# Optimization experiments

Measured on AMD Instinct MI355X. Metric: run time of the kernel, lower is better.

## Reference

```python
import jax, jax.numpy as jnp
import numpy as np

D = 256; NH = 8; NL = 4; NP = 4; HD = D // NH
SHAPES = np.array([[180, 180], [90, 90], [45, 45], [23, 23]], dtype=np.int32)
LQ = int((SHAPES[:, 0] * SHAPES[:, 1]).sum())  # 43054
STARTS = np.concatenate([[0], np.cumsum(SHAPES[:, 0] * SHAPES[:, 1])[:-1]]).astype(np.int32)


def setup_inputs():
    ks = jax.random.split(jax.random.key(0), 16)
    s = 0.02
    p = lambda k, shp: jax.random.normal(k, shp, jnp.float32) * s
    return {
        "query": jax.random.normal(ks[0], (1, LQ, D), jnp.float32),
        "ref_points": jax.random.uniform(ks[1], (1, LQ, NL, 2), dtype=jnp.float32),
        "pos": jax.random.normal(ks[2], (1, LQ, D), jnp.float32),
        "input_spatial_shapes": jnp.asarray(SHAPES),
        "input_level_start_index": jnp.asarray(STARTS),
        "w_off": p(ks[3], (D, NH * NL * NP * 2)), "b_off": p(ks[4], (NH * NL * NP * 2,)),
        "w_attn": p(ks[5], (D, NH * NL * NP)), "b_attn": p(ks[6], (NH * NL * NP,)),
        "w_val": p(ks[7], (D, D)), "b_val": jnp.zeros((D,), jnp.float32),
        "w_out": p(ks[8], (D, D)), "b_out": jnp.zeros((D,), jnp.float32),
        "g1": jnp.ones((D,), jnp.float32), "beta1": jnp.zeros((D,), jnp.float32),
        "w1": p(ks[9], (D, D)), "b1": jnp.zeros((D,), jnp.float32),
        "w2": p(ks[10], (D, D)), "b2": jnp.zeros((D,), jnp.float32),
        "g2": jnp.ones((D,), jnp.float32), "beta2": jnp.zeros((D,), jnp.float32),
    }


def _ln(x, g, b):
    m = x.mean(-1, keepdims=True)
    v = ((x - m) ** 2).mean(-1, keepdims=True)
    return (x - m) * jax.lax.rsqrt(v + 1e-5) * g + b


def _sample_level(v, Hl, Wl, loc):
    # v: (B, Hl*Wl, NH, HD); loc: (B, Lq, NH, NP, 2) normalized to [0,1]
    # Bilinear sampling matching F.grid_sample(align_corners=False, padding_mode='zeros')
    B, _, nh, d = v.shape
    Lq, P = loc.shape[1], loc.shape[3]
    vb = jnp.transpose(v, (0, 2, 1, 3))  # (B, NH, HW, d)
    x = loc[..., 0] * Wl - 0.5
    y = loc[..., 1] * Hl - 0.5
    x0 = jnp.floor(x); y0 = jnp.floor(y)
    fx = x - x0; fy = y - y0
    out = jnp.zeros((B, nh, Lq, P, d), v.dtype)
    for dy in (0, 1):
        for dx in (0, 1):
            xi = x0 + dx; yi = y0 + dy
            w = (fx if dx else 1.0 - fx) * (fy if dy else 1.0 - fy)
            valid = (xi >= 0) & (xi < Wl) & (yi >= 0) & (yi < Hl)
            xc = jnp.clip(xi, 0, Wl - 1).astype(jnp.int32)
            yc = jnp.clip(yi, 0, Hl - 1).astype(jnp.int32)
            idx = jnp.transpose(yc * Wl + xc, (0, 2, 1, 3)).reshape(B, nh, Lq * P)
            g = jnp.take_along_axis(vb, idx[..., None], axis=2).reshape(B, nh, Lq, P, d)
            wt = jnp.transpose(jnp.where(valid, w, 0.0), (0, 2, 1, 3))
            out = out + g * wt[..., None]
    return out  # (B, NH, Lq, NP, HD)


def _layer(query, ref_points, pos, shp, sti, w_off, b_off, w_attn, b_attn, w_val, b_val,
           w_out, b_out, g1, beta1, w1, b1, w2, b2, g2, beta2):
    B, Lq, _ = query.shape
    q = query + pos  # with_pos_embed
    value = (query @ w_val + b_val).reshape(B, Lq, NH, HD)
    off = (q @ w_off + b_off).reshape(B, Lq, NH, NL, NP, 2)
    aw = jax.nn.softmax((q @ w_attn + b_attn).reshape(B, Lq, NH, NL * NP), axis=-1)
    aw = aw.reshape(B, Lq, NH, NL, NP)
    # offset_normalizer = [W_l, H_l]
    norm = jnp.asarray(shp[:, ::-1].copy(), jnp.float32)
    loc = ref_points[:, :, None, :, None, :] + off / norm[None, None, None, :, None, :]
    acc = jnp.zeros((B, NH, Lq, HD), query.dtype)
    for l in range(NL):
        Hl, Wl = int(shp[l, 0]), int(shp[l, 1])
        st = int(sti[l])
        sampled = _sample_level(value[:, st:st + Hl * Wl], Hl, Wl, loc[:, :, :, l])
        wl = jnp.transpose(aw[:, :, :, l], (0, 2, 1, 3))  # (B, NH, Lq, NP)
        acc = acc + (sampled * wl[..., None]).sum(axis=3)
    attn_out = acc.transpose(0, 2, 1, 3).reshape(B, Lq, D) @ w_out + b_out
    # residual + LayerNorm + FFN (dropout is identity in eval mode)
    x = _ln(query + attn_out, g1, beta1)
    ffn = jax.nn.relu(x @ w1 + b1) @ w2 + b2
    return _ln(x + ffn, g2, beta2)


def reference(query, ref_points, pos, input_spatial_shapes, input_level_start_index,
              w_off, b_off, w_attn, b_attn, w_val, b_val, w_out, b_out,
              g1, beta1, w1, b1, w2, b2, g2, beta2):
    shp = np.asarray(input_spatial_shapes)
    sti = np.asarray(input_level_start_index)
    return _layer(query, ref_points, pos, shp, sti, w_off, b_off, w_attn, b_attn,
                  w_val, b_val, w_out, b_out, g1, beta1, w1, b1, w2, b2, g2, beta2)
```

## Files before the change

kernel.cpp:

```cpp
#include <hip/hip_runtime.h>

typedef unsigned short u16;
typedef unsigned int u32;
typedef float f32x4 __attribute__((ext_vector_type(4)));
typedef short i16x8 __attribute__((ext_vector_type(8)));
typedef __bf16 bf16x8_t __attribute__((ext_vector_type(8)));

#define LQ 43054

__device__ __forceinline__ float bf2f(u16 u) {
  union { u32 i; float f; } v; v.i = ((u32)u) << 16; return v.f;
}
__device__ __forceinline__ u16 f2bf(float f) {
  u32 i = __float_as_uint(f);
  return (u16)((i + 0x7FFFu + ((i >> 16) & 1u)) >> 16);
}

template <typename T>
__device__ __forceinline__ auto mfma_try(T a, T b, f32x4 c, int)
    -> decltype(__builtin_amdgcn_mfma_f32_16x16x32_bf16(a, b, c, 0, 0, 0)) {
  return __builtin_amdgcn_mfma_f32_16x16x32_bf16(a, b, c, 0, 0, 0);
}
template <typename T>
__device__ __forceinline__ f32x4 mfma_try(T a, T b, f32x4 c, long) {
  return __builtin_amdgcn_mfma_f32_16x16x32_bf16(
      __builtin_bit_cast(bf16x8_t, a), __builtin_bit_cast(bf16x8_t, b), c, 0, 0, 0);
}
__device__ __forceinline__ f32x4 mfma_bf16(i16x8 a, i16x8 b, f32x4 c) {
  return mfma_try(a, b, c, 0);
}

__global__ void transpose_all_kernel(
    const float* __restrict__ w_off, const float* __restrict__ w_attn,
    const float* __restrict__ w_val, const float* __restrict__ w_out,
    const float* __restrict__ w1, const float* __restrict__ w2,
    u16* __restrict__ wT) {
  int b = blockIdx.x;
  const float* src; u16* dst; int N; int col;
  if (b < 256)       { src = w_off;  dst = wT;          N = 256; col = b; }
  else if (b < 384)  { src = w_attn; dst = wT + 65536;  N = 128; col = b - 256; }
  else if (b < 640)  { src = w_val;  dst = wT + 98304;  N = 256; col = b - 384; }
  else if (b < 896)  { src = w_out;  dst = wT + 163840; N = 256; col = b - 640; }
  else if (b < 1152) { src = w1;     dst = wT + 229376; N = 256; col = b - 896; }
  else               { src = w2;     dst = wT + 294912; N = 256; col = b - 1152; }
  dst[col * 256 + threadIdx.x] = f2bf(src[threadIdx.x * N + col]);
}

__device__ __forceinline__ void stage_a_bf16(uint4* As, const u16* A, int r0, int M, int tid) {
#pragma unroll
  for (int it = 0; it < 8; ++it) {
    int e = tid + it * 256;
    int row = e >> 5, c = e & 31;
    int gr = r0 + row;
    uint4 v = make_uint4(0u, 0u, 0u, 0u);
    if (gr < M) v = ((const uint4*)A)[gr * 32 + c];
    As[row * 32 + (c ^ (row & 7))] = v;
  }
}
template <int ADD>
__device__ __forceinline__ void stage_a_f32(uint4* As, const float* A, const float* A2,
                                            int r0, int M, int tid) {
#pragma unroll
  for (int it = 0; it < 16; ++it) {
    int e = tid + it * 256;
    int row = e >> 6, c4 = e & 63;
    int gr = r0 + row;
    float4 v = make_float4(0.f, 0.f, 0.f, 0.f);
    if (gr < M) {
      v = ((const float4*)A)[gr * 64 + c4];
      if constexpr (ADD) {
        float4 p = ((const float4*)A2)[gr * 64 + c4];
        v.x += p.x; v.y += p.y; v.z += p.z; v.w += p.w;
      }
    }
    uint2 pk;
    pk.x = (u32)f2bf(v.x) | ((u32)f2bf(v.y) << 16);
    pk.y = (u32)f2bf(v.z) | ((u32)f2bf(v.w) << 16);
    int c = c4 >> 1, hf = c4 & 1;
    ((uint2*)As)[((row * 32 + (c ^ (row & 7))) << 1) | hf] = pk;
  }
}
__device__ __forceinline__ void load_b(i16x8* f, const u16* Bt, int t, int l16, int quad) {
  const uint4* bp = (const uint4*)Bt + (t * 16 + l16) * 32 + quad;
#pragma unroll
  for (int kk = 0; kk < 8; ++kk) f[kk] = __builtin_bit_cast(i16x8, bp[kk << 2]);
}
__device__ __forceinline__ void tile_mfma(f32x4* acc, const uint4* As,
                                          const i16x8* bfr, int l16, int quad) {
#pragma unroll
  for (int rg = 0; rg < 4; ++rg) {
    int arow = rg * 16 + l16;
    f32x4 a = {0.f, 0.f, 0.f, 0.f};
#pragma unroll
    for (int kk = 0; kk < 8; ++kk) {
      i16x8 afr = __builtin_bit_cast(i16x8, As[arow * 32 + (((kk << 2) + quad) ^ (arow & 7))]);
      a = mfma_bf16(afr, bfr[kk], a);
    }
    acc[rg] = a;
  }
}

#define LS_STRIDE 264
__device__ __forceinline__ void lds_store_rows(const u16* Ls, u16* out,
                                               int r0, int M, int w, int lane) {
#pragma unroll
  for (int it = 0; it < 8; ++it) {
    int lrow = w * 16 + it * 2 + (lane >> 5);
    int grow = r0 + lrow;
    int chunk = lane & 31;
    if (grow < M) {
      *(uint4*)(out + (size_t)grow * 256 + chunk * 8) =
          *(const uint4*)(Ls + lrow * LS_STRIDE + chunk * 8);
    }
  }
}

template <int AIN, int MODE, int NT>
__global__ __launch_bounds__(256, 3) void gemm_kernel(
    const void* __restrict__ Av, const u16* __restrict__ Bt,
    const float* __restrict__ bias, void* __restrict__ out, int M) {
  __shared__ uint4 As[2176];
  const int tid = threadIdx.x;
  const int w = tid >> 6, lane = tid & 63, quad = lane >> 4, l16 = lane & 15;
  const int r0 = blockIdx.x * 64;
  if constexpr (AIN == 2) stage_a_bf16(As, (const u16*)Av, r0, M, tid);
  else                    stage_a_f32<0>(As, (const float*)Av, nullptr, r0, M, tid);
  __syncthreads();
  i16x8 bfr[2][8];
  load_b(bfr[0], Bt, w * 4, l16, quad);
  f32x4 vals[4][4];
#pragma unroll
  for (int i = 0; i < 4; ++i) {
    const int t = w * 4 + i;
    if (i + 1 < 4) load_b(bfr[(i + 1) & 1], Bt, t + 1, l16, quad);
    tile_mfma(vals[i], As, bfr[i & 1], l16, quad);
  }
  __syncthreads();
  u16* Ls = (u16*)As;
#pragma unroll
  for (int i = 0; i < 4; ++i) {
    const int col = (w * 4 + i) * 16 + l16;
    const float bv = bias[col];
#pragma unroll
    for (int rg = 0; rg < 4; ++rg)
#pragma unroll
      for (int r = 0; r < 4; ++r) {
        float v = vals[i][rg][r] + bv;
        if (MODE == 2) v = fmaxf(v, 0.f);
        Ls[(rg * 16 + (quad << 2) + r) * LS_STRIDE + col] = f2bf(v);
      }
  }
  __syncthreads();
  lds_store_rows(Ls, (u16*)out, r0, M, w, lane);
}

__global__ __launch_bounds__(256, 3) void offaw_gemm_kernel(
    const float* __restrict__ query, const float* __restrict__ pos,
    const u16* __restrict__ Bt, const float* __restrict__ b_off,
    const float* __restrict__ b_attn, u16* __restrict__ offb,
    float* __restrict__ aw, int M) {
  __shared__ uint4 As[2176];
  const int tid = threadIdx.x;
  const int w = tid >> 6, lane = tid & 63, quad = lane >> 4, l16 = lane & 15;
  const int r0 = blockIdx.x * 64;
  stage_a_f32<1>(As, query, pos, r0, M, tid);
  __syncthreads();
  i16x8 bfr[2][8];
  load_b(bfr[0], Bt, w, l16, quad);
  f32x4 vals[4][4];
#pragma unroll
  for (int i = 0; i < 6; ++i) {
    const int t = w + 4 * i;
    if (i + 1 < 6) load_b(bfr[(i + 1) & 1], Bt, w + 4 * (i + 1), l16, quad);
    if (i < 4) {
      tile_mfma(vals[i], As, bfr[i & 1], l16, quad);
    } else {
      f32x4 acc[4];
      tile_mfma(acc, As, bfr[i & 1], l16, quad);
      const int colc = (t - 16) * 16 + l16;
      const float bv = b_attn[colc];
#pragma unroll
      for (int rg = 0; rg < 4; ++rg)
#pragma unroll
        for (int r = 0; r < 4; ++r) {
          float v = acc[rg][r] + bv;
          float m = v;
#pragma unroll
          for (int o = 1; o < 16; o <<= 1) m = fmaxf(m, __shfl_xor(m, o));
          float e = __expf(v - m);
          float s = e;
#pragma unroll
          for (int o = 1; o < 16; o <<= 1) s += __shfl_xor(s, o);
          int row = r0 + rg * 16 + (quad << 2) + r;
          if (row < M) aw[row * 128 + colc] = e / s;
        }
    }
  }
  __syncthreads();
  u16* Ls = (u16*)As;
#pragma unroll
  for (int i = 0; i < 4; ++i) {
    const int col = (w + 4 * i) * 16 + l16;
    const float bv = b_off[col];
#pragma unroll
    for (int rg = 0; rg < 4; ++rg)
#pragma unroll
      for (int r = 0; r < 4; ++r)
        Ls[(rg * 16 + (quad << 2) + r) * LS_STRIDE + col] = f2bf(vals[i][rg][r] + bv);
  }
  __syncthreads();
  lds_store_rows(Ls, offb, r0, M, w, lane);
}

template <int RBF, int OBF>
__global__ __launch_bounds__(256, 2) void gemm_ln_kernel(
    const u16* __restrict__ A, const u16* __restrict__ Bt,
    const float* __restrict__ bias, const void* __restrict__ residv,
    const float* __restrict__ g, const float* __restrict__ beta,
    void* __restrict__ outv, int M) {
  __shared__ uint4 As[2176];
  __shared__ float2 pnorm[256];
  const int tid = threadIdx.x;
  const int w = tid >> 6, lane = tid & 63, quad = lane >> 4, l16 = lane & 15;
  const int r0 = blockIdx.x * 64;
  stage_a_bf16(As, A, r0, M, tid);
  __syncthreads();
  i16x8 bfr[2][8];
  load_b(bfr[0], Bt, w * 4, l16, quad);
  f32x4 vals[4][4];
#pragma unroll
  for (int i = 0; i < 4; ++i) {
    const int t = w * 4 + i;
    if (i + 1 < 4) load_b(bfr[(i + 1) & 1], Bt, t + 1, l16, quad);
    tile_mfma(vals[i], As, bfr[i & 1], l16, quad);
  }
  float s[16], s2[16];
#pragma unroll
  for (int k = 0; k < 16; ++k) { s[k] = 0.f; s2[k] = 0.f; }
#pragma unroll
  for (int i = 0; i < 4; ++i) {
    const int col = (w * 4 + i) * 16 + l16;
    const float bv = bias[col];
#pragma unroll
    for (int rg = 0; rg < 4; ++rg)
#pragma unroll
      for (int r = 0; r < 4; ++r) {
        int row = r0 + rg * 16 + (quad << 2) + r;
        float rv = 0.f;
        if (row < M) rv = RBF ? bf2f(((const u16*)residv)[row * 256 + col])
                              : ((const float*)residv)[row * 256 + col];
        float v = vals[i][rg][r] + bv + rv;
        vals[i][rg][r] = v;
        s[rg * 4 + r] += v; s2[rg * 4 + r] += v * v;
      }
  }
#pragma unroll
  for (int k = 0; k < 16; ++k)
#pragma unroll
    for (int o = 1; o < 16; o <<= 1) {
      s[k] += __shfl_xor(s[k], o);
      s2[k] += __shfl_xor(s2[k], o);
    }
  if (l16 == 0) {
#pragma unroll
    for (int rg = 0; rg < 4; ++rg)
#pragma unroll
      for (int r = 0; r < 4; ++r) {
        int lrow = rg * 16 + (quad << 2) + r;
        pnorm[lrow * 4 + w] = make_float2(s[rg * 4 + r], s2[rg * 4 + r]);
      }
  }
  __syncthreads();
  if constexpr (OBF) {
    u16* Ls = (u16*)As;
#pragma unroll
    for (int rg = 0; rg < 4; ++rg)
#pragma unroll
      for (int r = 0; r < 4; ++r) {
        int lrow = rg * 16 + (quad << 2) + r;
        float4 p01 = ((const float4*)pnorm)[lrow * 2];
        float4 p23 = ((const float4*)pnorm)[lrow * 2 + 1];
        float ss = p01.x + p01.z + p23.x + p23.z;
        float qq = p01.y + p01.w + p23.y + p23.w;
        float mean = ss * (1.f / 256.f);
        float var = qq * (1.f / 256.f) - mean * mean;
        float inv = rsqrtf(var + 1e-5f);
#pragma unroll
        for (int i = 0; i < 4; ++i) {
          const int col = (w * 4 + i) * 16 + l16;
          float o = (vals[i][rg][r] - mean) * inv * g[col] + beta[col];
          Ls[lrow * LS_STRIDE + col] = f2bf(o);
        }
      }
    __syncthreads();
    lds_store_rows(Ls, (u16*)outv, r0, M, w, lane);
  } else {
#pragma unroll
    for (int rg = 0; rg < 4; ++rg)
#pragma unroll
      for (int r = 0; r < 4; ++r) {
        int lrow = rg * 16 + (quad << 2) + r;
        float4 p01 = ((const float4*)pnorm)[lrow * 2];
        float4 p23 = ((const float4*)pnorm)[lrow * 2 + 1];
        float ss = p01.x + p01.z + p23.x + p23.z;
        float qq = p01.y + p01.w + p23.y + p23.w;
        float mean = ss * (1.f / 256.f);
        float var = qq * (1.f / 256.f) - mean * mean;
        float inv = rsqrtf(var + 1e-5f);
        int row = r0 + lrow;
        if (row < M) {
#pragma unroll
          for (int i = 0; i < 4; ++i) {
            const int col = (w * 4 + i) * 16 + l16;
            float o = (vals[i][rg][r] - mean) * inv * g[col] + beta[col];
            ((float*)outv)[row * 256 + col] = o;
          }
        }
      }
  }
}

__global__ __launch_bounds__(256) void sampler_kernel(
    const float* __restrict__ refp, const u16* __restrict__ offb,
    const float* __restrict__ aw, const u16* __restrict__ value,
    u32* __restrict__ accv) {
  __shared__ uint4 rec[272];
  const int t = threadIdx.x;
  const int b = blockIdx.x;
  {
    const int qs = t >> 7, j = t & 127;
    const int i = b * 2 + qs;
    const int h = j >> 4, lp = j & 15, l = lp >> 2;
    const int Wl = (l == 0) ? 180 : (l == 1) ? 90 : (l == 2) ? 45 : 23;
    const int st = (l == 0) ? 0 : (l == 1) ? 32400 : (l == 2) ? 40500 : 42525;
    const float wj = aw[i * 128 + j];
    const u32 o2 = *(const u32*)(offb + i * 256 + h * 32 + lp * 2);
    const float ox = bf2f((u16)(o2 & 0xffffu)), oy = bf2f((u16)(o2 >> 16));
    const float rx = refp[i * 8 + l * 2], ry = refp[i * 8 + l * 2 + 1];
    float x = rx * (float)Wl + ox - 0.5f;
    float y = ry * (float)Wl + oy - 0.5f;
    float x0f = floorf(x), y0f = floorf(y);
    float fx = x - x0f, fy = y - y0f;
    int x0 = (int)x0f, y0 = (int)y0f;
    bool vx0 = (x0 >= 0) & (x0 < Wl), vx1 = (x0 + 1 >= 0) & (x0 + 1 < Wl);
    bool vy0 = (y0 >= 0) & (y0 < Wl), vy1 = (y0 + 1 >= 0) & (y0 + 1 < Wl);
    int x0c = min(max(x0, 0), Wl - 1), x1c = min(max(x0 + 1, 0), Wl - 1);
    int y0c = min(max(y0, 0), Wl - 1), y1c = min(max(y0 + 1, 0), Wl - 1);
    float w00 = (vx0 & vy0) ? wj * (1.f - fx) * (1.f - fy) : 0.f;
    float w01 = (vx1 & vy0) ? wj * fx * (1.f - fy) : 0.f;
    float w10 = (vx0 & vy1) ? wj * (1.f - fx) * fy : 0.f;
    float w11 = (vx1 & vy1) ? wj * fx * fy : 0.f;
    uint4 r;
    r.x = (u32)((st + y0c * Wl + x0c) * 512 + h * 64) | (u32)(x1c - x0c);
    r.y = (u32)(y1c - y0c) * (u32)(Wl * 512);
    r.z = (u32)f2bf(w00) | ((u32)f2bf(w01) << 16);
    r.w = (u32)f2bf(w10) | ((u32)f2bf(w11) << 16);
    rec[qs * 136 + h * 17 + lp] = r;
  }
  __syncthreads();
  const int qs = t >> 7, j = t & 127;
  const int h = j >> 4, dp = j & 15;
  const char* vb = (const char*)value;
  float a0 = 0.f, a1 = 0.f;
  const int rbase = qs * 136 + h * 17;
#pragma unroll
  for (int p = 0; p < 16; ++p) {
    uint4 r = rec[rbase + p];
    u32 base = (r.x & 0xFFFFFFFEu) + (u32)(dp * 4);
    u32 dxo = (r.x & 1u) << 9;
    u32 dyo = r.y;
    float w00 = __uint_as_float(r.z << 16);
    float w01 = __uint_as_float(r.z & 0xFFFF0000u);
    float w10 = __uint_as_float(r.w << 16);
    float w11 = __uint_as_float(r.w & 0xFFFF0000u);
    u32 p00 = *(const u32*)(vb + base);
    u32 p01 = *(const u32*)(vb + base + dxo);
    u32 p10 = *(const u32*)(vb + base + dyo);
    u32 p11 = *(const u32*)(vb + base + dyo + dxo);
    a0 = fmaf(w00, __uint_as_float(p00 << 16), a0);
    a1 = fmaf(w00, __uint_as_float(p00 & 0xFFFF0000u), a1);
    a0 = fmaf(w01, __uint_as_float(p01 << 16), a0);
    a1 = fmaf(w01, __uint_as_float(p01 & 0xFFFF0000u), a1);
    a0 = fmaf(w10, __uint_as_float(p10 << 16), a0);
    a1 = fmaf(w10, __uint_as_float(p10 & 0xFFFF0000u), a1);
    a0 = fmaf(w11, __uint_as_float(p11 << 16), a0);
    a1 = fmaf(w11, __uint_as_float(p11 & 0xFFFF0000u), a1);
  }
  u32 pk = (u32)f2bf(a0) | ((u32)f2bf(a1) << 16);
  accv[(b * 2 + qs) * 128 + j] = pk;
}

extern "C" void kernel_launch(void* const* d_in, const int* in_sizes, int n_in,
                              void* d_out, int out_size, void* d_ws, size_t ws_size,
                              hipStream_t stream) {
  const float* query  = (const float*)d_in[0];
  const float* refp   = (const float*)d_in[1];
  const float* pos    = (const float*)d_in[2];
  const float* w_off  = (const float*)d_in[5];
  const float* b_off  = (const float*)d_in[6];
  const float* w_attn = (const float*)d_in[7];
  const float* b_attn = (const float*)d_in[8];
  const float* w_val  = (const float*)d_in[9];
  const float* b_val  = (const float*)d_in[10];
  const float* w_out  = (const float*)d_in[11];
  const float* b_out  = (const float*)d_in[12];
  const float* g1     = (const float*)d_in[13];
  const float* beta1  = (const float*)d_in[14];
  const float* w1     = (const float*)d_in[15];
  const float* b1     = (const float*)d_in[16];
  const float* w2     = (const float*)d_in[17];
  const float* b2     = (const float*)d_in[18];
  const float* g2     = (const float*)d_in[19];
  const float* beta2  = (const float*)d_in[20];

  char* ws = (char*)d_ws;
  u16*   wT    = (u16*)(ws + 0);
  u16*   value = (u16*)(ws + 720896);
  u16*   offb  = (u16*)(ws + 22764544);
  float* aw    = (float*)(ws + 44808192);
  u16*   accb  = (u16*)(ws + 66851840);
  u16*   xb    = (u16*)(ws + 720896);
  u16*   hb    = (u16*)(ws + 22764544);

  u16* woffT  = wT;
  u16* wvalT  = wT + 98304;
  u16* woutT  = wT + 163840;
  u16* w1T    = wT + 229376;
  u16* w2T    = wT + 294912;

  transpose_all_kernel<<<1408, 256, 0, stream>>>(w_off, w_attn, w_val, w_out, w1, w2, wT);

  const int gm = (LQ + 63) / 64;
  gemm_kernel<0, 1, 4><<<gm, 256, 0, stream>>>(query, wvalT, b_val, value, LQ);
  offaw_gemm_kernel<<<gm, 256, 0, stream>>>(query, pos, woffT, b_off, b_attn, offb, aw, LQ);
  sampler_kernel<<<LQ / 2, 256, 0, stream>>>(refp, offb, aw, value, (u32*)accb);
  gemm_ln_kernel<0, 1><<<gm, 256, 0, stream>>>(accb, woutT, b_out, query, g1, beta1, xb, LQ);
  gemm_kernel<2, 2, 4><<<gm, 256, 0, stream>>>(xb, w1T, b1, hb, LQ);
  gemm_ln_kernel<1, 0><<<gm, 256, 0, stream>>>(hb, w2T, b2, xb, g2, beta2, d_out, LQ);
}
```

Before: 423.1 us.

## Use direct global-to-LDS loads, batch f32 staging loads, and dot2 bf16 sampling

The bf16 A-tile staging in the GEMM kernels now uses global_load_lds, which writes to shared memory without passing through registers. The swizzle is applied on the global address side, and out-of-range rows are clamped to the last row instead of zero-filled. The f32 staging path issues all loads of a phase before converting, so more loads are in flight at once. The sampler's bilinear accumulation now uses v_dot2_f32_bf16 with byte permutes instead of eight unpack-and-FMA steps per point. This trades some accumulation precision and adds reliance on the DMA path's layout matching the swizzle.

```diff
diff --git a/kernel.cpp b/kernel.cpp
--- a/kernel.cpp
+++ b/kernel.cpp
@@ -14,6 +14,12 @@
 __device__ __forceinline__ u16 f2bf(float f) {
   u32 i = __float_as_uint(f);
   return (u16)((i + 0x7FFFu + ((i >> 16) & 1u)) >> 16);
+}
+
+__device__ __forceinline__ float dot2bf(u32 v, u32 w, float c) {
+  float d;
+  asm("v_dot2_f32_bf16 %0, %1, %2, %3" : "=v"(d) : "v"(v), "v"(w), "v"(c));
+  return d;
 }
 
 template <typename T>
@@ -46,38 +52,50 @@
   dst[col * 256 + threadIdx.x] = f2bf(src[threadIdx.x * N + col]);
 }
 
-__device__ __forceinline__ void stage_a_bf16(uint4* As, const u16* A, int r0, int M, int tid) {
-#pragma unroll
-  for (int it = 0; it < 8; ++it) {
-    int e = tid + it * 256;
-    int row = e >> 5, c = e & 31;
-    int gr = r0 + row;
-    uint4 v = make_uint4(0u, 0u, 0u, 0u);
-    if (gr < M) v = ((const uint4*)A)[gr * 32 + c];
-    As[row * 32 + (c ^ (row & 7))] = v;
-  }
-}
-template <int ADD>
+__device__ __forceinline__ void stage_a_dma(uint4* As, const u16* A, int r0, int M,
+                                            int w, int lane) {
+#pragma unroll
+  for (int jj = 0; jj < 8; ++jj) {
+    int row = w * 16 + jj * 2 + (lane >> 5);
+    int gr = min(r0 + row, M - 1);
+    int c = lane & 31;
+    const uint4* gp = (const uint4*)A + (size_t)gr * 32 + (c ^ (row & 7));
+    __builtin_amdgcn_global_load_lds(
+        (const __attribute__((address_space(1))) void*)gp,
+        (__attribute__((address_space(3))) void*)(As + (w * 16 + jj * 2) * 32),
+        16, 0, 0);
+  }
+}
+template <int ADD, int PH>
 __device__ __forceinline__ void stage_a_f32(uint4* As, const float* A, const float* A2,
                                             int r0, int M, int tid) {
-#pragma unroll
-  for (int it = 0; it < 16; ++it) {
-    int e = tid + it * 256;
-    int row = e >> 6, c4 = e & 63;
-    int gr = r0 + row;
-    float4 v = make_float4(0.f, 0.f, 0.f, 0.f);
-    if (gr < M) {
-      v = ((const float4*)A)[gr * 64 + c4];
+  constexpr int IT = 16 / PH;
+#pragma unroll
+  for (int h = 0; h < PH; ++h) {
+    float4 va[IT];
+    float4 vp[ADD ? IT : 1];
+#pragma unroll
+    for (int it = 0; it < IT; ++it) {
+      int e = tid + (h * IT + it) * 256;
+      int gr = min(r0 + (e >> 6), M - 1);
+      int idx = gr * 64 + (e & 63);
+      va[it] = ((const float4*)A)[idx];
+      if constexpr (ADD) vp[it] = ((const float4*)A2)[idx];
+    }
+#pragma unroll
+    for (int it = 0; it < IT; ++it) {
+      int e = tid + (h * IT + it) * 256;
+      int row = e >> 6, c4 = e & 63;
+      float4 v = va[it];
       if constexpr (ADD) {
-        float4 p = ((const float4*)A2)[gr * 64 + c4];
-        v.x += p.x; v.y += p.y; v.z += p.z; v.w += p.w;
-      }
-    }
-    uint2 pk;
-    pk.x = (u32)f2bf(v.x) | ((u32)f2bf(v.y) << 16);
-    pk.y = (u32)f2bf(v.z) | ((u32)f2bf(v.w) << 16);
-    int c = c4 >> 1, hf = c4 & 1;
-    ((uint2*)As)[((row * 32 + (c ^ (row & 7))) << 1) | hf] = pk;
+        v.x += vp[it].x; v.y += vp[it].y; v.z += vp[it].z; v.w += vp[it].w;
+      }
+      uint2 pk;
+      pk.x = (u32)f2bf(v.x) | ((u32)f2bf(v.y) << 16);
+      pk.y = (u32)f2bf(v.z) | ((u32)f2bf(v.w) << 16);
+      int c = c4 >> 1, hf = c4 & 1;
+      ((uint2*)As)[((row * 32 + (c ^ (row & 7))) << 1) | hf] = pk;
+    }
   }
 }
 __device__ __forceinline__ void load_b(i16x8* f, const u16* Bt, int t, int l16, int quad) {
@@ -115,7 +133,7 @@
   }
 }
 
-template <int AIN, int MODE, int NT>
+template <int AIN, int MODE>
 __global__ __launch_bounds__(256, 3) void gemm_kernel(
     const void* __restrict__ Av, const u16* __restrict__ Bt,
     const float* __restrict__ bias, void* __restrict__ out, int M) {
@@ -123,8 +141,8 @@
   const int tid = threadIdx.x;
   const int w = tid >> 6, lane = tid & 63, quad = lane >> 4, l16 = lane & 15;
   const int r0 = blockIdx.x * 64;
-  if constexpr (AIN == 2) stage_a_bf16(As, (const u16*)Av, r0, M, tid);
-  else                    stage_a_f32<0>(As, (const float*)Av, nullptr, r0, M, tid);
+  if constexpr (AIN == 2) stage_a_dma(As, (const u16*)Av, r0, M, w, lane);
+  else                    stage_a_f32<0, 2>(As, (const float*)Av, nullptr, r0, M, tid);
   __syncthreads();
   i16x8 bfr[2][8];
   load_b(bfr[0], Bt, w * 4, l16, quad);
@@ -163,7 +181,7 @@
   const int tid = threadIdx.x;
   const int w = tid >> 6, lane = tid & 63, quad = lane >> 4, l16 = lane & 15;
   const int r0 = blockIdx.x * 64;
-  stage_a_f32<1>(As, query, pos, r0, M, tid);
+  stage_a_f32<1, 4>(As, query, pos, r0, M, tid);
   __syncthreads();
   i16x8 bfr[2][8];
   load_b(bfr[0], Bt, w, l16, quad);
@@ -223,7 +241,7 @@
   const int tid = threadIdx.x;
   const int w = tid >> 6, lane = tid & 63, quad = lane >> 4, l16 = lane & 15;
   const int r0 = blockIdx.x * 64;
-  stage_a_bf16(As, A, r0, M, tid);
+  stage_a_dma(As, A, r0, M, w, lane);
   __syncthreads();
   i16x8 bfr[2][8];
   load_b(bfr[0], Bt, w * 4, l16, quad);
@@ -363,28 +381,21 @@
   const char* vb = (const char*)value;
   float a0 = 0.f, a1 = 0.f;
   const int rbase = qs * 136 + h * 17;
+  const u32 dp4 = (u32)(dp * 4);
 #pragma unroll
   for (int p = 0; p < 16; ++p) {
     uint4 r = rec[rbase + p];
-    u32 base = (r.x & 0xFFFFFFFEu) + (u32)(dp * 4);
+    u32 base = (r.x & 0xFFFFFFFEu) + dp4;
     u32 dxo = (r.x & 1u) << 9;
     u32 dyo = r.y;
-    float w00 = __uint_as_float(r.z << 16);
-    float w01 = __uint_as_float(r.z & 0xFFFF0000u);
-    float w10 = __uint_as_float(r.w << 16);
-    float w11 = __uint_as_float(r.w & 0xFFFF0000u);
     u32 p00 = *(const u32*)(vb + base);
     u32 p01 = *(const u32*)(vb + base + dxo);
     u32 p10 = *(const u32*)(vb + base + dyo);
     u32 p11 = *(const u32*)(vb + base + dyo + dxo);
-    a0 = fmaf(w00, __uint_as_float(p00 << 16), a0);
-    a1 = fmaf(w00, __uint_as_float(p00 & 0xFFFF0000u), a1);
-    a0 = fmaf(w01, __uint_as_float(p01 << 16), a0);
-    a1 = fmaf(w01, __uint_as_float(p01 & 0xFFFF0000u), a1);
-    a0 = fmaf(w10, __uint_as_float(p10 << 16), a0);
-    a1 = fmaf(w10, __uint_as_float(p10 & 0xFFFF0000u), a1);
-    a0 = fmaf(w11, __uint_as_float(p11 << 16), a0);
-    a1 = fmaf(w11, __uint_as_float(p11 & 0xFFFF0000u), a1);
+    a0 = dot2bf(__builtin_amdgcn_perm(p01, p00, 0x05040100u), r.z, a0);
+    a1 = dot2bf(__builtin_amdgcn_perm(p01, p00, 0x07060302u), r.z, a1);
+    a0 = dot2bf(__builtin_amdgcn_perm(p11, p10, 0x05040100u), r.w, a0);
+    a1 = dot2bf(__builtin_amdgcn_perm(p11, p10, 0x07060302u), r.w, a1);
   }
   u32 pk = (u32)f2bf(a0) | ((u32)f2bf(a1) << 16);
   accv[(b * 2 + qs) * 128 + j] = pk;
@@ -431,10 +442,10 @@
   transpose_all_kernel<<<1408, 256, 0, stream>>>(w_off, w_attn, w_val, w_out, w1, w2, wT);
 
   const int gm = (LQ + 63) / 64;
-  gemm_kernel<0, 1, 4><<<gm, 256, 0, stream>>>(query, wvalT, b_val, value, LQ);
+  gemm_kernel<0, 1><<<gm, 256, 0, stream>>>(query, wvalT, b_val, value, LQ);
   offaw_gemm_kernel<<<gm, 256, 0, stream>>>(query, pos, woffT, b_off, b_attn, offb, aw, LQ);
   sampler_kernel<<<LQ / 2, 256, 0, stream>>>(refp, offb, aw, value, (u32*)accb);
   gemm_ln_kernel<0, 1><<<gm, 256, 0, stream>>>(accb, woutT, b_out, query, g1, beta1, xb, LQ);
-  gemm_kernel<2, 2, 4><<<gm, 256, 0, stream>>>(xb, w1T, b1, hb, LQ);
+  gemm_kernel<2, 2><<<gm, 256, 0, stream>>>(xb, w1T, b1, hb, LQ);
   gemm_ln_kernel<1, 0><<<gm, 256, 0, stream>>>(hb, w2T, b2, xb, g2, beta2, d_out, LQ);
 }
```

Result: no change. 419.3 us (-0.9%).
